# Kernel tuning notes

Hardware: AMD Instinct MI355X
Metric: run time of the kernel (lower is better)

Reference implementation:

```python
import jax, jax.numpy as jnp
import numpy as np

B, N, EMB, NCLS = 4, 4096, 1024, 13

def knn_euclid(x, k):
    # x: (B,C,N); k nearest by squared euclidean distance
    sq = jnp.sum(x * x, axis=1)                        # (B,N)
    inner = jnp.einsum('bcn,bcm->bnm', x, x)           # (B,N,N)
    d = sq[:, :, None] - 2.0 * inner + sq[:, None, :]
    return jax.lax.stop_gradient(jax.lax.top_k(-d, k)[1])   # (B,N,k)

def knn_cosine(x, k):
    xn = x / (jnp.linalg.norm(x, axis=1, keepdims=True) + 1e-8)
    sim = jnp.einsum('bcn,bcm->bnm', xn, xn)           # (B,N,N)
    return jax.lax.stop_gradient(jax.lax.top_k(sim, k)[1])

def edge_conv(x, idx, w0, s0, o0, w1, s1, o1):
    # x: (B,C,N), idx: (B,N,k) -> (B,64,N). Edge feats = concat(x_j - x_i, x_i).
    xt = jnp.transpose(x, (0, 2, 1))                   # (B,N,C)
    nbr = jax.vmap(lambda f, i: f[i])(xt, idx)         # (B,N,k,C)
    ctr = jnp.broadcast_to(xt[:, :, None, :], nbr.shape)
    e = jnp.concatenate([nbr - ctr, ctr], axis=-1)     # (B,N,k,2C)
    h = jax.nn.leaky_relu(jnp.einsum('bnkc,oc->bnko', e, w0) * s0 + o0, 0.2)
    h = jax.nn.leaky_relu(jnp.einsum('bnkc,oc->bnko', h, w1) * s1 + o1, 0.2)
    return jnp.transpose(jnp.max(h, axis=2), (0, 2, 1))  # max over k -> (B,64,N)

def conv1d(x, w):
    return jnp.einsum('bcn,oc->bon', x, w)

def setup_inputs():
    key = jax.random.key(0)
    cnt = [0]
    def nxt():
        cnt[0] += 1
        return jax.random.fold_in(key, cnt[0])
    W = lambda shape: jax.random.normal(nxt(), shape, jnp.float32) * 0.05
    S = lambda n: 1.0 + 0.1 * jax.random.normal(nxt(), (n,), jnp.float32)   # folded BN scale
    O = lambda n: 0.05 * jax.random.normal(nxt(), (n,), jnp.float32)        # folded BN offset / bias
    inp = {'x': jax.random.normal(nxt(), (B, 6, N), jnp.float32)}
    inp.update(w1_0=W((64, 12)), s1_0=S(64), o1_0=O(64), w1_1=W((64, 64)), s1_1=S(64), o1_1=O(64))
    inp.update(w2_0=W((64, 128)), s2_0=S(64), o2_0=O(64), w2_1=W((64, 64)), s2_1=S(64), o2_1=O(64))
    inp.update(w3_0=W((64, 128)), s3_0=S(64), o3_0=O(64), w3_1=W((64, 64)), s3_1=S(64), o3_1=O(64))
    inp.update(w4=W((EMB, 192)), b4=O(EMB))
    inp.update(wf1=W((512, EMB + 192)), sf1=S(512), of1=O(512))
    inp.update(wf2=W((256, 512)), sf2=S(256), of2=O(256))
    inp.update(wf3=W((NCLS, 256)))
    inp['k'] = 20
    return inp

def reference(x, w1_0, s1_0, o1_0, w1_1, s1_1, o1_1,
              w2_0, s2_0, o2_0, w2_1, s2_1, o2_1,
              w3_0, s3_0, o3_0, w3_1, s3_1, o3_1,
              w4, b4, wf1, sf1, of1, wf2, sf2, of2, wf3, k):
    x1 = edge_conv(x, knn_euclid(x, k), w1_0, s1_0, o1_0, w1_1, s1_1, o1_1)
    x2 = edge_conv(x1, knn_cosine(x1, k), w2_0, s2_0, o2_0, w2_1, s2_1, o2_1)
    x3 = edge_conv(x2, knn_cosine(x2, k), w3_0, s3_0, o3_0, w3_1, s3_1, o3_1)
    xc = jnp.concatenate([x1, x2, x3], axis=1)         # (B,192,N)
    x4 = jax.nn.leaky_relu(conv1d(xc, w4) + b4[None, :, None], 0.2)  # (B,EMB,N)
    g = jnp.max(x4, axis=2, keepdims=True)             # global max pool (B,EMB,1)
    g = jnp.broadcast_to(g, (x4.shape[0], x4.shape[1], xc.shape[2]))  # Repeat to N
    x5 = jnp.concatenate([x1, x2, x3, g], axis=1)      # (B,192+EMB,N)
    h = jax.nn.leaky_relu(conv1d(x5, wf1) * sf1[None, :, None] + of1[None, :, None], 0.2)
    h = jax.nn.leaky_relu(conv1d(h, wf2) * sf2[None, :, None] + of2[None, :, None], 0.2)
    return conv1d(h, wf3)                              # (B,NCLS,N)
```

## Files before the change

kernel.cpp:

```cpp
#include <hip/hip_runtime.h>
#include <hip/hip_bf16.h>
#include <float.h>

#define NPTS 4096
#define NB 4
#define KNN 20

typedef __attribute__((ext_vector_type(8))) short short8v;
typedef __attribute__((ext_vector_type(4))) float f32x4;
typedef unsigned long long u64;

#define MFMA_B16(acc, a, b) acc = __builtin_amdgcn_mfma_f32_16x16x32_bf16((a), (b), (acc), 0, 0, 0)

__device__ __forceinline__ float lrelu(float x) { return x > 0.f ? x : 0.2f * x; }

__device__ __forceinline__ void atomicMaxF(float* addr, float val) {
    int* ia = (int*)addr;
    int old = *ia;
    while (__int_as_float(old) < val) {
        int assumed = old;
        old = atomicCAS(ia, assumed, __float_as_int(val));
        if (old == assumed) break;
    }
}

__device__ __forceinline__ unsigned bf16rne(float x) {
    unsigned u = __float_as_uint(x);
    return (u + 0x7fffu + ((u >> 16) & 1u)) >> 16;
}

__device__ __forceinline__ unsigned sortkey_desc(float v) {
    unsigned u = __float_as_uint(v);
    unsigned s = (u & 0x80000000u) ? ~u : (u | 0x80000000u);
    return ~s;
}

__device__ __forceinline__ u64 bitonic64(u64 e, int ln) {
#pragma unroll
    for (int k = 2; k <= 64; k <<= 1) {
#pragma unroll
        for (int j = k >> 1; j > 0; j >>= 1) {
            u64 o = __shfl_xor(e, j);
            bool keepMin = (((ln & k) == 0) == ((ln & j) == 0));
            u64 mn = e < o ? e : o;
            u64 mx = e < o ? o : e;
            e = keepMin ? mn : mx;
        }
    }
    return e;
}

__device__ __forceinline__ void topk_merge(u64& topk, unsigned& thk, int& cnt,
                                           const u64* __restrict__ buf, int ln) {
    u64 e = (ln < 20) ? topk : ((ln - 20) < cnt ? buf[ln - 20] : ~0ull);
    e = bitonic64(e, ln);
    topk = e;
    u64 e19 = __shfl(e, 19);
    thk = (unsigned)(e19 >> 32);
    cnt = 0;
}

__global__ void k_transp(const float* __restrict__ src, float* __restrict__ dst,
                         int rows, int srcld, int cols) {
    int i = blockIdx.x * 256 + threadIdx.x;
    if (i >= rows * cols) return;
    int r = i % rows, c = i / rows;
    dst[c * rows + r] = src[(size_t)r * srcld + c];
}

__global__ void k_prep(const float* __restrict__ x, float* __restrict__ xpm8) {
    int i = blockIdx.x * 256 + threadIdx.x;
    int b = i >> 12, n = i & 4095;
    const float* xb = x + b * 6 * NPTS;
    float v[6]; float s = 0.f;
#pragma unroll
    for (int c = 0; c < 6; c++) { v[c] = xb[c * NPTS + n]; s += v[c] * v[c]; }
    float* o = xpm8 + (size_t)i * 8;
    *(float4*)(o)     = make_float4(v[0], v[1], v[2], v[3]);
    *(float4*)(o + 4) = make_float4(v[4], v[5], s, 0.f);
}

__global__ __launch_bounds__(256) void k_knn_euclid(const float* __restrict__ xpm8,
                                                    int* __restrict__ idx) {
    __shared__ u64 ebuf[4][44];
    int t = threadIdx.x;
    int w = t >> 6, ln = t & 63;
    int qid = blockIdx.x * 4 + w;
    int b = qid >> 12;
    const float* pb = xpm8 + (((size_t)b) << 12) * 8;
    const float* qp = xpm8 + (size_t)qid * 8;
    float4 qlo = *(const float4*)qp;
    float4 qhi = *(const float4*)(qp + 4);
    float sqn = qhi.z;
    u64 topk;
    unsigned thk;
    int cnt = 0;
    u64* bq = ebuf[w];
    {
        const float* cp = pb + ln * 8;
        float4 lo = *(const float4*)cp, hi = *(const float4*)(cp + 4);
        float dot = qlo.x * lo.x + qlo.y * lo.y + qlo.z * lo.z + qlo.w * lo.w
                  + qhi.x * hi.x + qhi.y * hi.y;
        float sv = -(sqn - 2.f * dot + hi.z);
        u64 e = ((u64)sortkey_desc(sv) << 32) | (unsigned)ln;
        e = bitonic64(e, ln);
        topk = e;
        thk = (unsigned)(__shfl(e, 19) >> 32);
    }
    for (int t0 = 64; t0 < NPTS; t0 += 64) {
        int m = t0 + ln;
        const float* cp = pb + (size_t)m * 8;
        float4 lo = *(const float4*)cp, hi = *(const float4*)(cp + 4);
        float dot = qlo.x * lo.x + qlo.y * lo.y + qlo.z * lo.z + qlo.w * lo.w
                  + qhi.x * hi.x + qhi.y * hi.y;
        float sv = -(sqn - 2.f * dot + hi.z);
        unsigned key = sortkey_desc(sv);
        bool pass = key < thk;
        u64 mask = __ballot(pass);
        if (!mask) continue;
        u64 key64 = ((u64)key << 32) | (unsigned)m;
        int cA = __popcll(mask & 0xFFFFFFFFull);
        int cB = __popcll(mask >> 32);
        if (cA) {
            if (cnt + cA > 44) topk_merge(topk, thk, cnt, bq, ln);
            if (pass && ln < 32) bq[cnt + __popcll(mask & ((1ull << ln) - 1))] = key64;
            cnt += cA;
        }
        if (cB) {
            if (cnt + cB > 44) topk_merge(topk, thk, cnt, bq, ln);
            if (pass && ln >= 32) bq[cnt + __popcll((mask >> 32) & ((1ull << (ln - 32)) - 1))] = key64;
            cnt += cB;
        }
    }
    if (cnt) topk_merge(topk, thk, cnt, bq, ln);
    if (ln < KNN) idx[qid * KNN + ln] = (int)(topk & 0xFFFFFFFFull);
}

__global__ __launch_bounds__(256) void k_knn_cos(const unsigned short* __restrict__ xsT,
                                                 int* __restrict__ idx) {
    __shared__ float simb[16][516];
    __shared__ u64 bufp[16][44];
    int t = threadIdx.x;
    int w = t >> 6, ln = t & 63;
    int b = blockIdx.x >> 8;
    int q0blk = (blockIdx.x & 255) * 16;
    int lp = ln & 15;
    const unsigned short* xsb = xsT + (size_t)b * 256 * 3072;
    const unsigned short* qtb = xsb + (size_t)(q0blk >> 4) * 3072 + ln * 8;
    short8v ah0 = *(const short8v*)(qtb);
    short8v ah1 = *(const short8v*)(qtb + 512);
    short8v am0 = *(const short8v*)(qtb + 1024);
    short8v am1 = *(const short8v*)(qtb + 1536);
    short8v al0 = *(const short8v*)(qtb + 2048);
    short8v al1 = *(const short8v*)(qtb + 2560);
    int myq = w * 4;
    u64 topk[4];
    unsigned thk[4];
    int cnt[4] = {0, 0, 0, 0};
    for (int strip = 0; strip < 8; strip++) {
        int tile0 = strip * 32 + w * 8;
        for (int tp = 0; tp < 4; tp++) {
            const unsigned short* tb0 = xsb + (size_t)(tile0 + tp * 2) * 3072 + ln * 8;
            const unsigned short* tb1 = tb0 + 3072;
            short8v bh0a = *(const short8v*)(tb0);
            short8v bh1a = *(const short8v*)(tb0 + 512);
            short8v bm0a = *(const short8v*)(tb0 + 1024);
            short8v bm1a = *(const short8v*)(tb0 + 1536);
            short8v bl0a = *(const short8v*)(tb0 + 2048);
            short8v bl1a = *(const short8v*)(tb0 + 2560);
            short8v bh0b = *(const short8v*)(tb1);
            short8v bh1b = *(const short8v*)(tb1 + 512);
            short8v bm0b = *(const short8v*)(tb1 + 1024);
            short8v bm1b = *(const short8v*)(tb1 + 1536);
            short8v bl0b = *(const short8v*)(tb1 + 2048);
            short8v bl1b = *(const short8v*)(tb1 + 2560);
            f32x4 p0 = {0.f, 0.f, 0.f, 0.f}, r0 = {0.f, 0.f, 0.f, 0.f};
            f32x4 p1 = {0.f, 0.f, 0.f, 0.f}, r1 = {0.f, 0.f, 0.f, 0.f};
            MFMA_B16(p0, ah0, bh0a); MFMA_B16(r0, ah1, bh1a);
            MFMA_B16(p1, ah0, bh0b); MFMA_B16(r1, ah1, bh1b);
            MFMA_B16(p0, ah0, bm0a); MFMA_B16(r0, ah1, bm1a);
            MFMA_B16(p1, ah0, bm0b); MFMA_B16(r1, ah1, bm1b);
            MFMA_B16(p0, am0, bh0a); MFMA_B16(r0, am1, bh1a);
            MFMA_B16(p1, am0, bh0b); MFMA_B16(r1, am1, bh1b);
            MFMA_B16(p0, ah0, bl0a); MFMA_B16(r0, ah1, bl1a);
            MFMA_B16(p1, ah0, bl0b); MFMA_B16(r1, ah1, bl1b);
            MFMA_B16(p0, al0, bh0a); MFMA_B16(r0, al1, bh1a);
            MFMA_B16(p1, al0, bh0b); MFMA_B16(r1, al1, bh1b);
            MFMA_B16(p0, am0, bm0a); MFMA_B16(r0, am1, bm1a);
            MFMA_B16(p1, am0, bm0b); MFMA_B16(r1, am1, bm1b);
            f32x4 s0 = p0 + r0;
            f32x4 s1 = p1 + r1;
            int row = (ln >> 4) * 4;
            int colL = w * 128 + tp * 32 + lp;
#pragma unroll
            for (int r = 0; r < 4; r++) {
                simb[row + r][colL] = s0[r];
                simb[row + r][colL + 16] = s1[r];
            }
        }
        __syncthreads();
#pragma unroll
        for (int q = 0; q < 4; q++) {
            u64* bq = bufp[myq + q];
            int j0 = 0;
            if (strip == 0) {
                float sv = simb[myq + q][ln];
                u64 e = ((u64)sortkey_desc(sv) << 32) | (unsigned)ln;
                e = bitonic64(e, ln);
                topk[q] = e;
                thk[q] = (unsigned)(__shfl(e, 19) >> 32);
                j0 = 1;
            }
            for (int j = j0; j < 8; j++) {
                float sv = simb[myq + q][j * 64 + ln];
                unsigned key = sortkey_desc(sv);
                bool pass = key < thk[q];
                u64 mask = __ballot(pass);
                if (!mask) continue;
                u64 key64 = ((u64)key << 32) | (unsigned)(strip * 512 + j * 64 + ln);
                int cA = __popcll(mask & 0xFFFFFFFFull);
                int cB = __popcll(mask >> 32);
                if (cA) {
                    if (cnt[q] + cA > 44) topk_merge(topk[q], thk[q], cnt[q], bq, ln);
                    if (pass && ln < 32) bq[cnt[q] + __popcll(mask & ((1ull << ln) - 1))] = key64;
                    cnt[q] += cA;
                }
                if (cB) {
                    if (cnt[q] + cB > 44) topk_merge(topk[q], thk[q], cnt[q], bq, ln);
                    if (pass && ln >= 32) bq[cnt[q] + __popcll((mask >> 32) & ((1ull << (ln - 32)) - 1))] = key64;
                    cnt[q] += cB;
                }
            }
        }
        __syncthreads();
    }
#pragma unroll
    for (int q = 0; q < 4; q++) {
        if (cnt[q]) topk_merge(topk[q], thk[q], cnt[q], bufp[myq + q], ln);
        if (ln < KNN) {
            int qid = (b << 12) + q0blk + myq + q;
            idx[(size_t)qid * KNN + ln] = (int)(topk[q] & 0xFFFFFFFFull);
        }
    }
}

__global__ void k_normalize(const float* __restrict__ xcpm, int coff,
                            unsigned short* __restrict__ xsT) {
    int pid = blockIdx.x * 256 + threadIdx.x;
    int b = pid >> 12, n = pid & 4095;
    const float* p = xcpm + (size_t)pid * 192 + coff;
    float s = 0.f;
#pragma unroll
    for (int c4 = 0; c4 < 16; c4++) {
        float4 v = *(const float4*)(p + c4 * 4);
        s += v.x * v.x + v.y * v.y + v.z * v.z + v.w * v.w;
    }
    float inv = 1.f / (sqrtf(s) + 1e-8f);
    unsigned short* q = xsT + (size_t)(b * 256 + (n >> 4)) * 3072 + (n & 15) * 8;
#pragma unroll
    for (int c4 = 0; c4 < 16; c4++) {
        float4 v = *(const float4*)(p + c4 * 4);
        float f[4] = {v.x * inv, v.y * inv, v.z * inv, v.w * inv};
        unsigned short hh[4], mm[4], ll[4];
#pragma unroll
        for (int j = 0; j < 4; j++) {
            float x = f[j];
            unsigned hb = bf16rne(x);
            float hf = __uint_as_float(hb << 16);
            float r1 = x - hf;
            unsigned mb = bf16rne(r1);
            float mf = __uint_as_float(mb << 16);
            float r2 = r1 - mf;
            unsigned lb = bf16rne(r2);
            hh[j] = (unsigned short)hb; mm[j] = (unsigned short)mb; ll[j] = (unsigned short)lb;
        }
        int h = c4 >> 3, kg = (c4 >> 1) & 3, off4 = (c4 & 1) * 4;
        int base = h * 512 + kg * 128 + off4;
        *(ushort4*)(q + base)        = make_ushort4(hh[0], hh[1], hh[2], hh[3]);
        *(ushort4*)(q + base + 1024) = make_ushort4(mm[0], mm[1], mm[2], mm[3]);
        *(ushort4*)(q + base + 2048) = make_ushort4(ll[0], ll[1], ll[2], ll[3]);
    }
}

__global__ __launch_bounds__(256) void k_edge1(const float* __restrict__ x,
    const float* __restrict__ w0, const float* __restrict__ s0, const float* __restrict__ o0,
    const float* __restrict__ w1, const float* __restrict__ s1, const float* __restrict__ o1,
    const int* __restrict__ idx, float* __restrict__ xcpm) {
    __shared__ float es[4][16];
    __shared__ float h0s[4][64];
    int t = threadIdx.x;
    int w = t >> 6, o = t & 63;
    int pid = blockIdx.x * 4 + w;
    int b = pid >> 12, n = pid & 4095;
    const float* xb = x + b * 6 * NPTS;
    float w0r[12];
    const float* w0p = w0 + o * 12;
#pragma unroll
    for (int c4 = 0; c4 < 3; c4++) {
        float4 v = *(const float4*)(w0p + c4 * 4);
        w0r[c4 * 4] = v.x; w0r[c4 * 4 + 1] = v.y; w0r[c4 * 4 + 2] = v.z; w0r[c4 * 4 + 3] = v.w;
    }
    float w1r[64];
    const float* w1p = w1 + o * 64;
#pragma unroll
    for (int c4 = 0; c4 < 16; c4++) {
        float4 v = *(const float4*)(w1p + c4 * 4);
        w1r[c4 * 4] = v.x; w1r[c4 * 4 + 1] = v.y; w1r[c4 * 4 + 2] = v.z; w1r[c4 * 4 + 3] = v.w;
    }
    float sv0 = s0[o], ov0 = o0[o], sv1 = s1[o], ov1 = o1[o];
    float cv = 0.f;
    if (o < 6) { cv = xb[o * NPTS + n]; es[w][6 + o] = cv; }
    if (o >= 12 && o < 16) es[w][o] = 0.f;
    float acc = -FLT_MAX;
    const int* ib = idx + pid * KNN;
    for (int kk = 0; kk < KNN; kk++) {
        int j = ib[kk] & 4095;
        if (o < 6) es[w][o] = xb[o * NPTS + j] - cv;
        float h = 0.f;
#pragma unroll
        for (int c4 = 0; c4 < 3; c4++) {
            float4 e4 = *(const float4*)&es[w][c4 * 4];
            h += w0r[c4 * 4] * e4.x + w0r[c4 * 4 + 1] * e4.y + w0r[c4 * 4 + 2] * e4.z + w0r[c4 * 4 + 3] * e4.w;
        }
        h = lrelu(h * sv0 + ov0);
        h0s[w][o] = h;
        float h2 = 0.f;
#pragma unroll
        for (int c4 = 0; c4 < 16; c4++) {
            float4 h4 = *(const float4*)&h0s[w][c4 * 4];
            h2 += w1r[c4 * 4] * h4.x + w1r[c4 * 4 + 1] * h4.y + w1r[c4 * 4 + 2] * h4.z + w1r[c4 * 4 + 3] * h4.w;
        }
        h2 = lrelu(h2 * sv1 + ov1);
        acc = fmaxf(acc, h2);
    }
    xcpm[(size_t)pid * 192 + o] = acc;
}

__global__ __launch_bounds__(256) void k_edge23(const float* __restrict__ xcpm,
    const float* __restrict__ w0, const float* __restrict__ s0, const float* __restrict__ o0,
    const float* __restrict__ w1, const float* __restrict__ s1, const float* __restrict__ o1,
    const int* __restrict__ idx, int ci, int co) {
    __shared__ float cs[4][64];
    __shared__ float es[4][64];
    __shared__ float h0s[4][64];
    int t = threadIdx.x;
    int w = t >> 6, o = t & 63;
    int pid = blockIdx.x * 4 + w;
    int b = pid >> 12;
    float w0r[64];
    const float* w0p = w0 + o * 128;
#pragma unroll
    for (int c4 = 0; c4 < 16; c4++) {
        float4 v = *(const float4*)(w0p + c4 * 4);
        w0r[c4 * 4] = v.x; w0r[c4 * 4 + 1] = v.y; w0r[c4 * 4 + 2] = v.z; w0r[c4 * 4 + 3] = v.w;
    }
    float w1r[64];
    const float* w1p = w1 + o * 64;
#pragma unroll
    for (int c4 = 0; c4 < 16; c4++) {
        float4 v = *(const float4*)(w1p + c4 * 4);
        w1r[c4 * 4] = v.x; w1r[c4 * 4 + 1] = v.y; w1r[c4 * 4 + 2] = v.z; w1r[c4 * 4 + 3] = v.w;
    }
    float sv0 = s0[o], ov0 = o0[o], sv1 = s1[o], ov1 = o1[o];
    float cv = xcpm[(size_t)pid * 192 + ci + o];
    cs[w][o] = cv;
    float h0b = 0.f;
    const float* w0q = w0p + 64;
#pragma unroll
    for (int c4 = 0; c4 < 16; c4++) {
        float4 wv = *(const float4*)(w0q + c4 * 4);
        float4 c4v = *(const float4*)&cs[w][c4 * 4];
        h0b += wv.x * c4v.x + wv.y * c4v.y + wv.z * c4v.z + wv.w * c4v.w;
    }
    float acc = -FLT_MAX;
    const int* ib = idx + pid * KNN;
    int j0 = ib[0] & 4095;
    float nv = xcpm[((size_t)(b * 4096 + j0)) * 192 + ci + o];
    for (int kk = 0; kk < KNN; kk++) {
        float cur = nv;
        if (kk < KNN - 1) {
            int jn = ib[kk + 1] & 4095;
            nv = xcpm[((size_t)(b * 4096 + jn)) * 192 + ci + o];
        }
        es[w][o] = cur - cv;
        float h = h0b;
#pragma unroll
        for (int c4 = 0; c4 < 16; c4++) {
            float4 e4 = *(const float4*)&es[w][c4 * 4];
            h += w0r[c4 * 4] * e4.x + w0r[c4 * 4 + 1] * e4.y + w0r[c4 * 4 + 2] * e4.z + w0r[c4 * 4 + 3] * e4.w;
        }
        h = lrelu(h * sv0 + ov0);
        h0s[w][o] = h;
        float h2 = 0.f;
#pragma unroll
        for (int c4 = 0; c4 < 16; c4++) {
            float4 h4 = *(const float4*)&h0s[w][c4 * 4];
            h2 += w1r[c4 * 4] * h4.x + w1r[c4 * 4 + 1] * h4.y + w1r[c4 * 4 + 2] * h4.z + w1r[c4 * 4 + 3] * h4.w;
        }
        h2 = lrelu(h2 * sv1 + ov1);
        acc = fmaxf(acc, h2);
    }
    float* outp = (float*)xcpm;
    outp[(size_t)pid * 192 + co + o] = acc;
}

__global__ void k_init_g(float* __restrict__ g) {
    g[blockIdx.x * 256 + threadIdx.x] = -FLT_MAX;
}

__global__ __launch_bounds__(256) void k_w4pool(const float* __restrict__ xc,
                                                const float* __restrict__ wT4,
                                                const float* __restrict__ b4,
                                                float* __restrict__ g) {
    __shared__ float xcs[192 * 68];
    int t = threadIdx.x;
    int b = blockIdx.y;
    int n0 = blockIdx.x * 64;
    const float* xb = xc + (size_t)(b * 4096 + n0) * 192;
    for (int i = t; i < 3072; i += 256) {
        int pt = i / 48, c4 = i - pt * 48;
        float4 v = *(const float4*)(xb + pt * 192 + c4 * 4);
        xcs[(c4 * 4 + 0) * 68 + pt] = v.x; xcs[(c4 * 4 + 1) * 68 + pt] = v.y;
        xcs[(c4 * 4 + 2) * 68 + pt] = v.z; xcs[(c4 * 4 + 3) * 68 + pt] = v.w;
    }
    __syncthreads();
    int o0 = (t >> 2) * 16, qd = t & 3;
    float4 bb[4];
#pragma unroll
    for (int k = 0; k < 4; k++) bb[k] = *(const float4*)(b4 + o0 + k * 4);
    float mx[16];
#pragma unroll
    for (int oo = 0; oo < 16; oo++) mx[oo] = -FLT_MAX;
    for (int sub = 0; sub < 4; sub++) {
        int tn0 = sub * 16 + qd * 4;
        float4 acc[16];
#pragma unroll
        for (int oo = 0; oo < 16; oo++) acc[oo] = (float4){0, 0, 0, 0};
        for (int c = 0; c < 192; c++) {
            float4 x4 = *(const float4*)&xcs[c * 68 + tn0];
            const float* wr = wT4 + c * 1024 + o0;
            float4 wq[4];
#pragma unroll
            for (int k = 0; k < 4; k++) wq[k] = *(const float4*)(wr + k * 4);
#pragma unroll
            for (int oo = 0; oo < 16; oo++) {
                float wv = ((const float*)wq)[oo];
                acc[oo].x += wv * x4.x; acc[oo].y += wv * x4.y;
                acc[oo].z += wv * x4.z; acc[oo].w += wv * x4.w;
            }
        }
#pragma unroll
        for (int oo = 0; oo < 16; oo++) {
            float bias = ((const float*)bb)[oo];
            float4 a = acc[oo];
            float h = fmaxf(fmaxf(lrelu(a.x + bias), lrelu(a.y + bias)),
                            fmaxf(lrelu(a.z + bias), lrelu(a.w + bias)));
            mx[oo] = fmaxf(mx[oo], h);
        }
    }
#pragma unroll
    for (int oo = 0; oo < 16; oo++) {
        float v = mx[oo];
        v = fmaxf(v, __shfl_xor(v, 1));
        v = fmaxf(v, __shfl_xor(v, 2));
        if (qd == 0) atomicMaxF(&g[b * 1024 + o0 + oo], v);
    }
}

__global__ __launch_bounds__(256) void k_goff(const float* __restrict__ g,
                                              const float* __restrict__ wf1,
                                              const float* __restrict__ sf1,
                                              const float* __restrict__ of1,
                                              float* __restrict__ goff) {
    int bo = blockIdx.x;
    int b = bo >> 9, o = bo & 511;
    int t = threadIdx.x;
    const float* wr = wf1 + (size_t)o * 1216 + 192;
    const float* gb = g + b * 1024;
    float s = 0.f;
    for (int c = t; c < 1024; c += 256) s += wr[c] * gb[c];
    __shared__ float red[4];
    for (int off = 32; off > 0; off >>= 1) s += __shfl_down(s, off);
    if ((t & 63) == 0) red[t >> 6] = s;
    __syncthreads();
    if (t == 0) {
        float tot = red[0] + red[1] + red[2] + red[3];
        goff[bo] = tot * sf1[o] + of1[o];
    }
}

#define TP 20
__global__ __launch_bounds__(256) void k_tail(const float* __restrict__ xc,
                                              const float* __restrict__ wf1T,
                                              const float* __restrict__ sf1,
                                              const float* __restrict__ goff,
                                              const float* __restrict__ wf2T,
                                              const float* __restrict__ sf2,
                                              const float* __restrict__ of2,
                                              const float* __restrict__ wf3,
                                              float* __restrict__ out) {
    __shared__ float xcs[192 * TP];
    __shared__ float h1s[512 * TP];
    __shared__ float h2s[256 * TP];
    int t = threadIdx.x;
    int b = blockIdx.y;
    int n0 = blockIdx.x * 16;
    const float* xb = xc + (size_t)(b * 4096 + n0) * 192;
    for (int i = t; i < 768; i += 256) {
        int pt = i / 48, c4 = i - pt * 48;
        float4 v = *(const float4*)(xb + pt * 192 + c4 * 4);
        xcs[(c4 * 4 + 0) * TP + pt] = v.x; xcs[(c4 * 4 + 1) * TP + pt] = v.y;
        xcs[(c4 * 4 + 2) * TP + pt] = v.z; xcs[(c4 * 4 + 3) * TP + pt] = v.w;
    }
    __syncthreads();
    {
        int o8 = (t >> 2) * 8, tn0 = (t & 3) * 4;
        float4 acc[8];
#pragma unroll
        for (int oo = 0; oo < 8; oo++) acc[oo] = (float4){0, 0, 0, 0};
        for (int c = 0; c < 192; c++) {
            float4 x4 = *(const float4*)&xcs[c * TP + tn0];
            const float* wr = wf1T + c * 512 + o8;
            float4 w0 = *(const float4*)(wr);
            float4 w1 = *(const float4*)(wr + 4);
            float wq[8] = {w0.x, w0.y, w0.z, w0.w, w1.x, w1.y, w1.z, w1.w};
#pragma unroll
            for (int oo = 0; oo < 8; oo++) {
                acc[oo].x += wq[oo] * x4.x; acc[oo].y += wq[oo] * x4.y;
                acc[oo].z += wq[oo] * x4.z; acc[oo].w += wq[oo] * x4.w;
            }
        }
#pragma unroll
        for (int oo = 0; oo < 8; oo++) {
            int o = o8 + oo;
            float s = sf1[o];
            float gv = goff[b * 512 + o];
            float4 r;
            r.x = lrelu(acc[oo].x * s + gv); r.y = lrelu(acc[oo].y * s + gv);
            r.z = lrelu(acc[oo].z * s + gv); r.w = lrelu(acc[oo].w * s + gv);
            *(float4*)&h1s[o * TP + tn0] = r;
        }
    }
    __syncthreads();
    {
        int o4 = (t >> 2) * 4, tn0 = (t & 3) * 4;
        float4 acc[4];
#pragma unroll
        for (int oo = 0; oo < 4; oo++) acc[oo] = (float4){0, 0, 0, 0};
        for (int c = 0; c < 512; c++) {
            float4 x4 = *(const float4*)&h1s[c * TP + tn0];
            float4 w = *(const float4*)(wf2T + c * 256 + o4);
            float wq[4] = {w.x, w.y, w.z, w.w};
#pragma unroll
            for (int oo = 0; oo < 4; oo++) {
                acc[oo].x += wq[oo] * x4.x; acc[oo].y += wq[oo] * x4.y;
                acc[oo].z += wq[oo] * x4.z; acc[oo].w += wq[oo] * x4.w;
            }
        }
#pragma unroll
        for (int oo = 0; oo < 4; oo++) {
            int o = o4 + oo;
            float s = sf2[o], of = of2[o];
            float4 r;
            r.x = lrelu(acc[oo].x * s + of); r.y = lrelu(acc[oo].y * s + of);
            r.z = lrelu(acc[oo].z * s + of); r.w = lrelu(acc[oo].w * s + of);
            *(float4*)&h2s[o * TP + tn0] = r;
        }
    }
    __syncthreads();
    if (t < 13 * 16) {
        int o = t >> 4, tn = t & 15;
        const float* wr = wf3 + o * 256;
        float acc = 0.f;
        for (int c4 = 0; c4 < 64; c4++) {
            float4 wv = *(const float4*)(wr + c4 * 4);
            acc += wv.x * h2s[(c4 * 4 + 0) * TP + tn] + wv.y * h2s[(c4 * 4 + 1) * TP + tn]
                 + wv.z * h2s[(c4 * 4 + 2) * TP + tn] + wv.w * h2s[(c4 * 4 + 3) * TP + tn];
        }
        out[((size_t)b * 13 + o) * NPTS + n0 + tn] = acc;
    }
}

extern "C" void kernel_launch(void* const* d_in, const int* in_sizes, int n_in,
                              void* d_out, int out_size, void* d_ws, size_t ws_size,
                              hipStream_t stream) {
    const float* x    = (const float*)d_in[0];
    const float* w1_0 = (const float*)d_in[1];
    const float* s1_0 = (const float*)d_in[2];
    const float* o1_0 = (const float*)d_in[3];
    const float* w1_1 = (const float*)d_in[4];
    const float* s1_1 = (const float*)d_in[5];
    const float* o1_1 = (const float*)d_in[6];
    const float* w2_0 = (const float*)d_in[7];
    const float* s2_0 = (const float*)d_in[8];
    const float* o2_0 = (const float*)d_in[9];
    const float* w2_1 = (const float*)d_in[10];
    const float* s2_1 = (const float*)d_in[11];
    const float* o2_1 = (const float*)d_in[12];
    const float* w3_0 = (const float*)d_in[13];
    const float* s3_0 = (const float*)d_in[14];
    const float* o3_0 = (const float*)d_in[15];
    const float* w3_1 = (const float*)d_in[16];
    const float* s3_1 = (const float*)d_in[17];
    const float* o3_1 = (const float*)d_in[18];
    const float* w4   = (const float*)d_in[19];
    const float* b4   = (const float*)d_in[20];
    const float* wf1  = (const float*)d_in[21];
    const float* sf1  = (const float*)d_in[22];
    const float* of1  = (const float*)d_in[23];
    const float* wf2  = (const float*)d_in[24];
    const float* sf2  = (const float*)d_in[25];
    const float* of2  = (const float*)d_in[26];
    const float* wf3  = (const float*)d_in[27];

    float* xcpm = (float*)d_ws;
    float* xpm8 = xcpm + (size_t)NB * NPTS * 192;
    float* g    = xpm8 + (size_t)NB * NPTS * 8;
    float* goff = g + NB * 1024;
    int*   idx  = (int*)(goff + NB * 512);
    float* wT4  = (float*)(idx + NB * NPTS * KNN);
    float* wf1T = wT4 + 192 * 1024;
    float* wf2T = wf1T + 192 * 512;
    unsigned short* xsT = (unsigned short*)(wf2T + 512 * 256);
    (void)in_sizes; (void)n_in; (void)out_size; (void)ws_size;

    k_transp<<<(1024 * 192 + 255) / 256, 256, 0, stream>>>(w4, wT4, 1024, 192, 192);
    k_transp<<<(512 * 192 + 255) / 256, 256, 0, stream>>>(wf1, wf1T, 512, 1216, 192);
    k_transp<<<(256 * 512 + 255) / 256, 256, 0, stream>>>(wf2, wf2T, 256, 512, 512);
    k_prep<<<NB * NPTS / 256, 256, 0, stream>>>(x, xpm8);
    k_knn_euclid<<<NB * NPTS / 4, 256, 0, stream>>>(xpm8, idx);
    k_edge1<<<NB * NPTS / 4, 256, 0, stream>>>(x, w1_0, s1_0, o1_0, w1_1, s1_1, o1_1, idx, xcpm);
    k_normalize<<<NB * NPTS / 256, 256, 0, stream>>>(xcpm, 0, xsT);
    k_knn_cos<<<NB * NPTS / 16, 256, 0, stream>>>(xsT, idx);
    k_edge23<<<NB * NPTS / 4, 256, 0, stream>>>(xcpm, w2_0, s2_0, o2_0, w2_1, s2_1, o2_1, idx, 0, 64);
    k_normalize<<<NB * NPTS / 256, 256, 0, stream>>>(xcpm, 64, xsT);
    k_knn_cos<<<NB * NPTS / 16, 256, 0, stream>>>(xsT, idx);
    k_edge23<<<NB * NPTS / 4, 256, 0, stream>>>(xcpm, w3_0, s3_0, o3_0, w3_1, s3_1, o3_1, idx, 64, 128);
    k_init_g<<<NB * 1024 / 256, 256, 0, stream>>>(g);
    k_w4pool<<<dim3(NPTS / 64, NB), 256, 0, stream>>>(xcpm, wT4, b4, g);
    k_goff<<<NB * 512, 256, 0, stream>>>(g, wf1, sf1, of1, goff);
    k_tail<<<dim3(NPTS / 16, NB), 256, 0, stream>>>(xcpm, wf1T, sf1, goff, wf2T, sf2, of2, wf3, (float*)d_out);
}
```

Before: 1.422 ms.

## Process 32 queries per block in cosine kNN and batch edge-conv over neighbours

The cosine kNN kernel now computes a 32-query by 256-candidate similarity strip per block (two query tiles held in registers), so each loaded candidate tile feeds twice as many MFMAs and global loads of candidate tiles are halved. Each wave now handles 8 queries' top-k selection. The edge-conv kernel for layers 2 and 3 gathers all 20 neighbour differences into shared memory up front and computes both MLP layers for all neighbours at once. Weights are streamed per channel chunk instead of held as 128 registers. This removes the serial per-neighbour gather latency, at the cost of larger shared memory and register pressure from 20-wide accumulator arrays.

```diff
diff --git a/kernel.cpp b/kernel.cpp
--- a/kernel.cpp
+++ b/kernel.cpp
@@ -11,6 +11,14 @@
 typedef unsigned long long u64;
 
 #define MFMA_B16(acc, a, b) acc = __builtin_amdgcn_mfma_f32_16x16x32_bf16((a), (b), (acc), 0, 0, 0)
+
+#define SIM6(P, R, A, B) \
+    MFMA_B16(P, A[0], B[0]); MFMA_B16(R, A[1], B[1]); \
+    MFMA_B16(P, A[0], B[2]); MFMA_B16(R, A[1], B[3]); \
+    MFMA_B16(P, A[2], B[0]); MFMA_B16(R, A[3], B[1]); \
+    MFMA_B16(P, A[0], B[4]); MFMA_B16(R, A[1], B[5]); \
+    MFMA_B16(P, A[4], B[0]); MFMA_B16(R, A[5], B[1]); \
+    MFMA_B16(P, A[2], B[2]); MFMA_B16(R, A[3], B[3]);
 
 __device__ __forceinline__ float lrelu(float x) { return x > 0.f ? x : 0.2f * x; }
 
@@ -138,86 +146,76 @@
 
 __global__ __launch_bounds__(256) void k_knn_cos(const unsigned short* __restrict__ xsT,
                                                  int* __restrict__ idx) {
-    __shared__ float simb[16][516];
-    __shared__ u64 bufp[16][44];
+    __shared__ float simb[32][260];
+    __shared__ u64 bufp[32][44];
     int t = threadIdx.x;
     int w = t >> 6, ln = t & 63;
-    int b = blockIdx.x >> 8;
-    int q0blk = (blockIdx.x & 255) * 16;
+    int b = blockIdx.x >> 7;
+    int q0blk = (blockIdx.x & 127) * 32;
     int lp = ln & 15;
     const unsigned short* xsb = xsT + (size_t)b * 256 * 3072;
-    const unsigned short* qtb = xsb + (size_t)(q0blk >> 4) * 3072 + ln * 8;
-    short8v ah0 = *(const short8v*)(qtb);
-    short8v ah1 = *(const short8v*)(qtb + 512);
-    short8v am0 = *(const short8v*)(qtb + 1024);
-    short8v am1 = *(const short8v*)(qtb + 1536);
-    short8v al0 = *(const short8v*)(qtb + 2048);
-    short8v al1 = *(const short8v*)(qtb + 2560);
-    int myq = w * 4;
-    u64 topk[4];
-    unsigned thk[4];
-    int cnt[4] = {0, 0, 0, 0};
-    for (int strip = 0; strip < 8; strip++) {
-        int tile0 = strip * 32 + w * 8;
-        for (int tp = 0; tp < 4; tp++) {
-            const unsigned short* tb0 = xsb + (size_t)(tile0 + tp * 2) * 3072 + ln * 8;
+    const unsigned short* qt0 = xsb + (size_t)(q0blk >> 4) * 3072 + ln * 8;
+    const unsigned short* qt1 = qt0 + 3072;
+    short8v A0[6], A1[6];
+#pragma unroll
+    for (int p = 0; p < 6; p++) {
+        A0[p] = *(const short8v*)(qt0 + p * 512);
+        A1[p] = *(const short8v*)(qt1 + p * 512);
+    }
+    u64 topk[8];
+    unsigned thk[8];
+    int cnt[8] = {0, 0, 0, 0, 0, 0, 0, 0};
+    for (int strip = 0; strip < 16; strip++) {
+#pragma unroll
+        for (int tp = 0; tp < 2; tp++) {
+            int tt0 = w * 4 + tp * 2;
+            const unsigned short* tb0 = xsb + (size_t)(strip * 16 + tt0) * 3072 + ln * 8;
             const unsigned short* tb1 = tb0 + 3072;
-            short8v bh0a = *(const short8v*)(tb0);
-            short8v bh1a = *(const short8v*)(tb0 + 512);
-            short8v bm0a = *(const short8v*)(tb0 + 1024);
-            short8v bm1a = *(const short8v*)(tb0 + 1536);
-            short8v bl0a = *(const short8v*)(tb0 + 2048);
-            short8v bl1a = *(const short8v*)(tb0 + 2560);
-            short8v bh0b = *(const short8v*)(tb1);
-            short8v bh1b = *(const short8v*)(tb1 + 512);
-            short8v bm0b = *(const short8v*)(tb1 + 1024);
-            short8v bm1b = *(const short8v*)(tb1 + 1536);
-            short8v bl0b = *(const short8v*)(tb1 + 2048);
-            short8v bl1b = *(const short8v*)(tb1 + 2560);
-            f32x4 p0 = {0.f, 0.f, 0.f, 0.f}, r0 = {0.f, 0.f, 0.f, 0.f};
-            f32x4 p1 = {0.f, 0.f, 0.f, 0.f}, r1 = {0.f, 0.f, 0.f, 0.f};
-            MFMA_B16(p0, ah0, bh0a); MFMA_B16(r0, ah1, bh1a);
-            MFMA_B16(p1, ah0, bh0b); MFMA_B16(r1, ah1, bh1b);
-            MFMA_B16(p0, ah0, bm0a); MFMA_B16(r0, ah1, bm1a);
-            MFMA_B16(p1, ah0, bm0b); MFMA_B16(r1, ah1, bm1b);
-            MFMA_B16(p0, am0, bh0a); MFMA_B16(r0, am1, bh1a);
-            MFMA_B16(p1, am0, bh0b); MFMA_B16(r1, am1, bh1b);
-            MFMA_B16(p0, ah0, bl0a); MFMA_B16(r0, ah1, bl1a);
-            MFMA_B16(p1, ah0, bl0b); MFMA_B16(r1, ah1, bl1b);
-            MFMA_B16(p0, al0, bh0a); MFMA_B16(r0, al1, bh1a);
-            MFMA_B16(p1, al0, bh0b); MFMA_B16(r1, al1, bh1b);
-            MFMA_B16(p0, am0, bm0a); MFMA_B16(r0, am1, bm1a);
-            MFMA_B16(p1, am0, bm0b); MFMA_B16(r1, am1, bm1b);
-            f32x4 s0 = p0 + r0;
-            f32x4 s1 = p1 + r1;
+            short8v Ba[6], Bb[6];
+#pragma unroll
+            for (int p = 0; p < 6; p++) {
+                Ba[p] = *(const short8v*)(tb0 + p * 512);
+                Bb[p] = *(const short8v*)(tb1 + p * 512);
+            }
+            f32x4 p00 = {0.f,0.f,0.f,0.f}, r00 = {0.f,0.f,0.f,0.f};
+            f32x4 p01 = {0.f,0.f,0.f,0.f}, r01 = {0.f,0.f,0.f,0.f};
+            f32x4 p10 = {0.f,0.f,0.f,0.f}, r10 = {0.f,0.f,0.f,0.f};
+            f32x4 p11 = {0.f,0.f,0.f,0.f}, r11 = {0.f,0.f,0.f,0.f};
+            SIM6(p00, r00, A0, Ba); SIM6(p01, r01, A0, Bb);
+            SIM6(p10, r10, A1, Ba); SIM6(p11, r11, A1, Bb);
+            f32x4 s00 = p00 + r00, s01 = p01 + r01;
+            f32x4 s10 = p10 + r10, s11 = p11 + r11;
             int row = (ln >> 4) * 4;
-            int colL = w * 128 + tp * 32 + lp;
+            int colL = tt0 * 16 + lp;
 #pragma unroll
             for (int r = 0; r < 4; r++) {
-                simb[row + r][colL] = s0[r];
-                simb[row + r][colL + 16] = s1[r];
+                simb[row + r][colL]           = s00[r];
+                simb[row + r][colL + 16]      = s01[r];
+                simb[16 + row + r][colL]      = s10[r];
+                simb[16 + row + r][colL + 16] = s11[r];
             }
         }
         __syncthreads();
 #pragma unroll
-        for (int q = 0; q < 4; q++) {
-            u64* bq = bufp[myq + q];
+        for (int q = 0; q < 8; q++) {
+            int lq = w * 8 + q;
+            u64* bq = bufp[lq];
             int j0 = 0;
             if (strip == 0) {
-                float sv = simb[myq + q][ln];
+                float sv = simb[lq][ln];
                 u64 e = ((u64)sortkey_desc(sv) << 32) | (unsigned)ln;
                 e = bitonic64(e, ln);
                 topk[q] = e;
                 thk[q] = (unsigned)(__shfl(e, 19) >> 32);
                 j0 = 1;
             }
-            for (int j = j0; j < 8; j++) {
-                float sv = simb[myq + q][j * 64 + ln];
+            for (int j = j0; j < 4; j++) {
+                float sv = simb[lq][j * 64 + ln];
                 unsigned key = sortkey_desc(sv);
                 bool pass = key < thk[q];
                 u64 mask = __ballot(pass);
                 if (!mask) continue;
-                u64 key64 = ((u64)key << 32) | (unsigned)(strip * 512 + j * 64 + ln);
+                u64 key64 = ((u64)key << 32) | (unsigned)(strip * 256 + j * 64 + ln);
                 int cA = __popcll(mask & 0xFFFFFFFFull);
                 int cB = __popcll(mask >> 32);
                 if (cA) {
@@ -235,10 +233,11 @@
         __syncthreads();
     }
 #pragma unroll
-    for (int q = 0; q < 4; q++) {
-        if (cnt[q]) topk_merge(topk[q], thk[q], cnt[q], bufp[myq + q], ln);
+    for (int q = 0; q < 8; q++) {
+        int lq = w * 8 + q;
+        if (cnt[q]) topk_merge(topk[q], thk[q], cnt[q], bufp[lq], ln);
         if (ln < KNN) {
-            int qid = (b << 12) + q0blk + myq + q;
+            int qid = (b << 12) + q0blk + lq;
             idx[(size_t)qid * KNN + ln] = (int)(topk[q] & 0xFFFFFFFFull);
         }
     }
@@ -341,65 +340,62 @@
     const float* __restrict__ w1, const float* __restrict__ s1, const float* __restrict__ o1,
     const int* __restrict__ idx, int ci, int co) {
     __shared__ float cs[4][64];
-    __shared__ float es[4][64];
-    __shared__ float h0s[4][64];
+    __shared__ float es[4][KNN][64];
+    __shared__ float h0s[4][KNN][64];
     int t = threadIdx.x;
     int w = t >> 6, o = t & 63;
     int pid = blockIdx.x * 4 + w;
     int b = pid >> 12;
-    float w0r[64];
-    const float* w0p = w0 + o * 128;
-#pragma unroll
-    for (int c4 = 0; c4 < 16; c4++) {
-        float4 v = *(const float4*)(w0p + c4 * 4);
-        w0r[c4 * 4] = v.x; w0r[c4 * 4 + 1] = v.y; w0r[c4 * 4 + 2] = v.z; w0r[c4 * 4 + 3] = v.w;
-    }
-    float w1r[64];
-    const float* w1p = w1 + o * 64;
-#pragma unroll
-    for (int c4 = 0; c4 < 16; c4++) {
-        float4 v = *(const float4*)(w1p + c4 * 4);
-        w1r[c4 * 4] = v.x; w1r[c4 * 4 + 1] = v.y; w1r[c4 * 4 + 2] = v.z; w1r[c4 * 4 + 3] = v.w;
-    }
     float sv0 = s0[o], ov0 = o0[o], sv1 = s1[o], ov1 = o1[o];
     float cv = xcpm[(size_t)pid * 192 + ci + o];
     cs[w][o] = cv;
-    float h0b = 0.f;
-    const float* w0q = w0p + 64;
-#pragma unroll
+    const int* ib = idx + pid * KNN;
+    const float* xb = xcpm + ((size_t)(b * 4096)) * 192 + ci;
+#pragma unroll
+    for (int j = 0; j < KNN; j++) {
+        int jn = ib[j] & 4095;
+        es[w][j][o] = xb[(size_t)jn * 192 + o] - cv;
+    }
+    const float* w0p = w0 + o * 128;
+    float h0b;
+    {
+        float hb[4] = {0.f, 0.f, 0.f, 0.f};
+#pragma unroll
+        for (int c4 = 0; c4 < 16; c4++) {
+            float4 wv = *(const float4*)(w0p + 64 + c4 * 4);
+            float4 c4v = *(const float4*)&cs[w][c4 * 4];
+            hb[c4 & 3] += wv.x * c4v.x + wv.y * c4v.y + wv.z * c4v.z + wv.w * c4v.w;
+        }
+        h0b = (hb[0] + hb[1]) + (hb[2] + hb[3]);
+    }
+    float h0a[KNN];
+#pragma unroll
+    for (int j = 0; j < KNN; j++) h0a[j] = h0b;
     for (int c4 = 0; c4 < 16; c4++) {
-        float4 wv = *(const float4*)(w0q + c4 * 4);
-        float4 c4v = *(const float4*)&cs[w][c4 * 4];
-        h0b += wv.x * c4v.x + wv.y * c4v.y + wv.z * c4v.z + wv.w * c4v.w;
+        float4 wv = *(const float4*)(w0p + c4 * 4);
+#pragma unroll
+        for (int j = 0; j < KNN; j++) {
+            float4 e = *(const float4*)&es[w][j][c4 * 4];
+            h0a[j] += wv.x * e.x + wv.y * e.y + wv.z * e.z + wv.w * e.w;
+        }
+    }
+#pragma unroll
+    for (int j = 0; j < KNN; j++) h0s[w][j][o] = lrelu(h0a[j] * sv0 + ov0);
+    const float* w1p = w1 + o * 64;
+    float h1a[KNN];
+#pragma unroll
+    for (int j = 0; j < KNN; j++) h1a[j] = 0.f;
+    for (int c4 = 0; c4 < 16; c4++) {
+        float4 wv = *(const float4*)(w1p + c4 * 4);
+#pragma unroll
+        for (int j = 0; j < KNN; j++) {
+            float4 e = *(const float4*)&h0s[w][j][c4 * 4];
+            h1a[j] += wv.x * e.x + wv.y * e.y + wv.z * e.z + wv.w * e.w;
+        }
     }
     float acc = -FLT_MAX;
-    const int* ib = idx + pid * KNN;
-    int j0 = ib[0] & 4095;
-    float nv = xcpm[((size_t)(b * 4096 + j0)) * 192 + ci + o];
-    for (int kk = 0; kk < KNN; kk++) {
-        float cur = nv;
-        if (kk < KNN - 1) {
-            int jn = ib[kk + 1] & 4095;
-            nv = xcpm[((size_t)(b * 4096 + jn)) * 192 + ci + o];
-        }
-        es[w][o] = cur - cv;
-        float h = h0b;
-#pragma unroll
-        for (int c4 = 0; c4 < 16; c4++) {
-            float4 e4 = *(const float4*)&es[w][c4 * 4];
-            h += w0r[c4 * 4] * e4.x + w0r[c4 * 4 + 1] * e4.y + w0r[c4 * 4 + 2] * e4.z + w0r[c4 * 4 + 3] * e4.w;
-        }
-        h = lrelu(h * sv0 + ov0);
-        h0s[w][o] = h;
-        float h2 = 0.f;
-#pragma unroll
-        for (int c4 = 0; c4 < 16; c4++) {
-            float4 h4 = *(const float4*)&h0s[w][c4 * 4];
-            h2 += w1r[c4 * 4] * h4.x + w1r[c4 * 4 + 1] * h4.y + w1r[c4 * 4 + 2] * h4.z + w1r[c4 * 4 + 3] * h4.w;
-        }
-        h2 = lrelu(h2 * sv1 + ov1);
-        acc = fmaxf(acc, h2);
-    }
+#pragma unroll
+    for (int j = 0; j < KNN; j++) acc = fmaxf(acc, lrelu(h1a[j] * sv1 + ov1));
     float* outp = (float*)xcpm;
     outp[(size_t)pid * 192 + co + o] = acc;
 }
@@ -631,10 +627,10 @@
     k_knn_euclid<<<NB * NPTS / 4, 256, 0, stream>>>(xpm8, idx);
     k_edge1<<<NB * NPTS / 4, 256, 0, stream>>>(x, w1_0, s1_0, o1_0, w1_1, s1_1, o1_1, idx, xcpm);
     k_normalize<<<NB * NPTS / 256, 256, 0, stream>>>(xcpm, 0, xsT);
-    k_knn_cos<<<NB * NPTS / 16, 256, 0, stream>>>(xsT, idx);
+    k_knn_cos<<<NB * NPTS / 32, 256, 0, stream>>>(xsT, idx);
     k_edge23<<<NB * NPTS / 4, 256, 0, stream>>>(xcpm, w2_0, s2_0, o2_0, w2_1, s2_1, o2_1, idx, 0, 64);
     k_normalize<<<NB * NPTS / 256, 256, 0, stream>>>(xcpm, 64, xsT);
-    k_knn_cos<<<NB * NPTS / 16, 256, 0, stream>>>(xsT, idx);
+    k_knn_cos<<<NB * NPTS / 32, 256, 0, stream>>>(xsT, idx);
     k_edge23<<<NB * NPTS / 4, 256, 0, stream>>>(xcpm, w3_0, s3_0, o3_0, w3_1, s3_1, o3_1, idx, 64, 128);
     k_init_g<<<NB * 1024 / 256, 256, 0, stream>>>(g);
     k_w4pool<<<dim3(NPTS / 64, NB), 256, 0, stream>>>(xcpm, wT4, b4, g);
```

Measured after the change: 1.283 ms. 1.11x faster.
